# Performance work log

Hardware: AMD Instinct MI355X
Metric: run time of the kernel (lower is better)

Reference implementation:

```python
import jax, jax.numpy as jnp
import numpy as np

T, N, F_IN, F_HID, E = 12, 10000, 128, 128, 160000


def _gcn_norm(src, dst, ew, n):
    # PyG gcn_norm with add_self_loops=False: deg from edge_weight scattered at dst
    deg = jnp.zeros((n,), ew.dtype).at[dst].add(ew)
    dinv = jnp.where(deg > 0, jax.lax.rsqrt(jnp.where(deg > 0, deg, 1.0)), 0.0)
    return dinv[src] * ew * dinv[dst]


def _gcn(x, W, b, src, dst, norm, n):
    h = x @ W                                   # [n, out]
    out = jnp.zeros((n, W.shape[1]), h.dtype).at[dst].add(norm[:, None] * h[src])
    return out + b


def setup_inputs() -> dict:
    key = jax.random.key(0)
    ks = jax.random.split(key, 8)
    s = 1.0 / np.sqrt(F_IN)
    return {
        "x": jax.random.normal(ks[0], (T, N, F_IN), jnp.float32),
        "edge_index": jax.random.randint(ks[1], (2, E), 0, N, dtype=jnp.int64),
        "edge_weight": jax.random.uniform(ks[2], (E,), jnp.float32),
        "W1": jax.random.normal(ks[3], (F_IN, F_HID), jnp.float32) * s,
        "b1": jnp.zeros((F_HID,), jnp.float32),
        "W2": jax.random.normal(ks[4], (F_HID, F_IN), jnp.float32) * s,
        "b2": jnp.zeros((F_IN,), jnp.float32),
        "Wt1": jax.random.normal(ks[5], (F_IN, F_HID), jnp.float32) * s,
        "bt1": jnp.zeros((F_HID,), jnp.float32),
        "Wt2": jax.random.normal(ks[6], (F_HID, F_IN), jnp.float32) * s,
        "bt2": jnp.zeros((F_IN,), jnp.float32),
    }


def reference(x, edge_index, edge_weight, W1, b1, W2, b2, Wt1, bt1, Wt2, bt2):
    src, dst = edge_index[0], edge_index[1]
    norm = _gcn_norm(src, dst, edge_weight, N)

    def spatial(xt):  # [N, F_IN]
        h = jax.nn.relu(_gcn(xt, W1, b1, src, dst, norm, N))
        return _gcn(h, W2, b2, src, dst, norm, N)

    x = jax.vmap(spatial)(x)                    # [T, N, F_IN]

    # temporal block: bidirectional chain edges between consecutive time steps
    xf = x.reshape(T * N, F_IN)
    fwd = jnp.arange((T - 1) * N)
    tsrc = jnp.concatenate([fwd, fwd + N])
    tdst = jnp.concatenate([fwd + N, fwd])
    tw = jnp.ones(tsrc.shape, xf.dtype)
    tnorm = _gcn_norm(tsrc, tdst, tw, T * N)
    h = jax.nn.relu(_gcn(xf, Wt1, bt1, tsrc, tdst, tnorm, T * N))
    xf = _gcn(h, Wt2, bt2, tsrc, tdst, tnorm, T * N)
    x = xf.reshape(T, N, F_IN)

    return jnp.tanh(x)
```

## Files before the change

kernel.cpp:

```cpp
#include <hip/hip_runtime.h>
#include <hip/hip_bf16.h>
#include <hip/hip_fp16.h>

#define T_STEPS 12
#define N_NODES 10000
#define FDIM 128
#define M_ROWS (T_STEPS * N_NODES)

typedef __attribute__((ext_vector_type(8))) short short8v;
typedef __attribute__((ext_vector_type(8))) _Float16 half8v;
typedef __attribute__((ext_vector_type(2))) _Float16 half2v;
typedef __attribute__((ext_vector_type(4))) float f32x4;


__global__ __launch_bounds__(256) void k_count(const int* __restrict__ ei, int* __restrict__ cnt, int E) {
    int e = blockIdx.x * 256 + threadIdx.x;
    if (e < E) atomicAdd(&cnt[ei[E + e]], 1);
}

__global__ __launch_bounds__(1024) void k_scan(const int* __restrict__ cnt, int* __restrict__ rowptr,
                                               int* __restrict__ cursor) {
    __shared__ int buf[1024];
    __shared__ int base_s;
    int tid = threadIdx.x;
    if (tid == 0) base_s = 0;
    __syncthreads();
    for (int c0 = 0; c0 < N_NODES; c0 += 1024) {
        int i = c0 + tid;
        int x = (i < N_NODES) ? cnt[i] : 0;
        buf[tid] = x;
        __syncthreads();
        for (int off = 1; off < 1024; off <<= 1) {
            int v = (tid >= off) ? buf[tid - off] : 0;
            __syncthreads();
            buf[tid] += v;
            __syncthreads();
        }
        int excl = base_s + buf[tid] - x;
        if (i < N_NODES) { rowptr[i] = excl; cursor[i] = excl; }
        __syncthreads();
        if (tid == 0) base_s = base_s + buf[1023];
        __syncthreads();
    }
    if (tid == 0) rowptr[N_NODES] = base_s;
}

__global__ __launch_bounds__(256) void k_fill(const int* __restrict__ ei, const float* __restrict__ ew,
                                              int* __restrict__ cursor, uint2* __restrict__ epack, int E) {
    int e = blockIdx.x * 256 + threadIdx.x;
    if (e < E) {
        int s = ei[e];
        int d = ei[E + e];
        int slot = atomicAdd(&cursor[d], 1);
        epack[slot] = make_uint2((unsigned)s, __builtin_bit_cast(unsigned, ew[e]));
    }
}

__global__ __launch_bounds__(256) void k_dinv(const int* __restrict__ rowptr, const uint2* __restrict__ epack,
                                              float* __restrict__ dinv) {
    int n = blockIdx.x * 256 + threadIdx.x;
    if (n < N_NODES) {
        int r0 = rowptr[n], r1 = rowptr[n + 1];
        float s = 0.f;
        for (int i = r0; i < r1; ++i) s += __builtin_bit_cast(float, epack[i].y);
        dinv[n] = (s > 0.f) ? rsqrtf(s) : 0.f;
    }
}

__global__ __launch_bounds__(256) void k_scale(const int* __restrict__ rowptr, uint2* __restrict__ epack,
                                               const float* __restrict__ dinv) {
    int n = blockIdx.x * 256 + threadIdx.x;
    if (n < N_NODES) {
        int r0 = rowptr[n], r1 = rowptr[n + 1];
        float dn = dinv[n];
        for (int i = r0; i < r1; ++i) {
            uint2 e = epack[i];
            float v = dn * __builtin_bit_cast(float, e.y) * dinv[e.x];
            epack[i] = make_uint2(e.x * 256u, __builtin_bit_cast(unsigned, v));
        }
    }
}


__global__ __launch_bounds__(256) void k_wsplit4(const float* __restrict__ Wa, const float* __restrict__ Wb,
                                                 const float* __restrict__ Wc, const float* __restrict__ Wd,
                                                 short* __restrict__ base) {
    int wsel = blockIdx.y;
    const float* W = (wsel == 0) ? Wa : (wsel == 1) ? Wb : (wsel == 2) ? Wc : Wd;
    short* Whf = base + (size_t)wsel * 2 * FDIM * FDIM;
    short* Wlf = Whf + FDIM * FDIM;
    int idx = blockIdx.x * 256 + threadIdx.x;
    int k = idx >> 7, col = idx & 127;
    int s = k >> 5, kb = (k >> 3) & 3, j = k & 7;
    float w = W[(size_t)k * FDIM + col];
    _Float16 hi = (_Float16)w;
    _Float16 lo = (_Float16)(w - (float)hi);
    size_t oi = (size_t)(((s * 4 + kb) * 128 + col)) * 8 + j;
    Whf[oi] = __builtin_bit_cast(short, hi);
    Wlf[oi] = __builtin_bit_cast(short, lo);
}


template <typename IN_T, typename OUT_T>
__global__ __launch_bounds__(256) void k_gemm_f16(const IN_T* __restrict__ A,
                                                  const short* __restrict__ Whf,
                                                  const short* __restrict__ Wlf,
                                                  OUT_T* __restrict__ C, int Mrows) {
    int tid = threadIdx.x;
    int wave = tid >> 6, lane = tid & 63;
    int lr = lane & 15, kb = lane >> 4;
    int rbase = blockIdx.x * 128 + wave * 32;

    f32x4 acc[2][8];
#pragma unroll
    for (int m = 0; m < 2; ++m)
#pragma unroll
        for (int n = 0; n < 8; ++n) acc[m][n] = (f32x4){0.f, 0.f, 0.f, 0.f};

#pragma unroll
    for (int s = 0; s < 4; ++s) {
        half8v a[2];
#pragma unroll
        for (int m = 0; m < 2; ++m) {
            int r = rbase + m * 16 + lr;
            if (r > Mrows - 1) r = Mrows - 1;
            const IN_T* ap = &A[(size_t)r * FDIM + s * 32 + kb * 8];
            if constexpr (sizeof(IN_T) == 4) {
                float4 x0 = *(const float4*)ap;
                float4 x1 = *(const float4*)(ap + 4);
                a[m][0] = (_Float16)x0.x; a[m][1] = (_Float16)x0.y;
                a[m][2] = (_Float16)x0.z; a[m][3] = (_Float16)x0.w;
                a[m][4] = (_Float16)x1.x; a[m][5] = (_Float16)x1.y;
                a[m][6] = (_Float16)x1.z; a[m][7] = (_Float16)x1.w;
            } else {
                a[m] = __builtin_bit_cast(half8v, *(const short8v*)ap);
            }
        }
#pragma unroll
        for (int n = 0; n < 8; ++n) {
            size_t wo = (size_t)(((s * 4 + kb) * 128 + n * 16 + lr)) * 8;
            half8v wh = __builtin_bit_cast(half8v, *(const short8v*)&Whf[wo]);
            half8v wl = __builtin_bit_cast(half8v, *(const short8v*)&Wlf[wo]);
#pragma unroll
            for (int m = 0; m < 2; ++m) {
                acc[m][n] = __builtin_amdgcn_mfma_f32_16x16x32_f16(a[m], wh, acc[m][n], 0, 0, 0);
                acc[m][n] = __builtin_amdgcn_mfma_f32_16x16x32_f16(a[m], wl, acc[m][n], 0, 0, 0);
            }
        }
    }
#pragma unroll
    for (int m = 0; m < 2; ++m)
#pragma unroll
        for (int q = 0; q < 4; ++q) {
            int r = rbase + m * 16 + kb * 4 + q;
            if (r < Mrows) {
#pragma unroll
                for (int n = 0; n < 8; ++n)
                    C[(size_t)r * FDIM + n * 16 + lr] = (OUT_T)acc[m][n][q];
            }
        }
}


#define NPB 20
#define NB_HALF 250

__global__ __launch_bounds__(128) void k_aggx(const char* __restrict__ Sbytes,
                                              const int* __restrict__ rowptr,
                                              const uint2* __restrict__ epack,
                                              const float* __restrict__ bias, __half* __restrict__ out,
                                              int do_relu) {
    int bid = blockIdx.x;
    int x = bid & 7;
    int j = bid >> 3;
    int unit = j / NB_HALF;
    int nb = j - unit * NB_HALF;
    int t, n0;
    if (unit == 2) { t = 8 + (x >> 1); n0 = (x & 1) * 5000 + nb * NPB; }
    else           { t = x;            n0 = unit * 5000 + nb * NPB; }

    int wave = threadIdx.x >> 6, lane = threadIdx.x & 63;
    const char* St = Sbytes + (size_t)t * N_NODES * 256;
    unsigned lane4 = (unsigned)lane * 4u;
    float b0 = bias[2 * lane], b1 = bias[2 * lane + 1];

    int nbase = n0 + wave * (NPB / 2);
    for (int nn = 0; nn < NPB / 2; ++nn) {
        int n = nbase + nn;
        int r0 = __builtin_amdgcn_readfirstlane(rowptr[n]);
        int r1 = __builtin_amdgcn_readfirstlane(rowptr[n + 1]);
        float a0 = 0.f, a1 = 0.f;
        int i = r0;
        while (i + 16 <= r1) {
            unsigned sx[16]; float sv[16];
#pragma unroll
            for (int q = 0; q < 16; ++q) {
                uint2 e = epack[i + q];
                sx[q] = e.x;
                sv[q] = __builtin_bit_cast(float, e.y);
            }
            unsigned u[16];
#pragma unroll
            for (int q = 0; q < 16; ++q)
                u[q] = *(const unsigned*)(St + (sx[q] + lane4));
#pragma unroll
            for (int q = 0; q < 16; ++q) {
                half2v h = __builtin_bit_cast(half2v, u[q]);
                a0 = fmaf(sv[q], (float)h[0], a0);
                a1 = fmaf(sv[q], (float)h[1], a1);
            }
            i += 16;
        }
        while (i < r1) {
            unsigned sx[8]; float sv[8];
#pragma unroll
            for (int q = 0; q < 8; ++q) {
                int ii = i + q;
                int ic = (ii < r1) ? ii : r1 - 1;
                uint2 e = epack[ic];
                sx[q] = e.x;
                sv[q] = (ii < r1) ? __builtin_bit_cast(float, e.y) : 0.f;
            }
            unsigned u[8];
#pragma unroll
            for (int q = 0; q < 8; ++q)
                u[q] = *(const unsigned*)(St + (sx[q] + lane4));
#pragma unroll
            for (int q = 0; q < 8; ++q) {
                half2v h = __builtin_bit_cast(half2v, u[q]);
                a0 = fmaf(sv[q], (float)h[0], a0);
                a1 = fmaf(sv[q], (float)h[1], a1);
            }
            i += 8;
        }
        float o0 = a0 + b0, o1 = a1 + b1;
        if (do_relu) { o0 = fmaxf(o0, 0.f); o1 = fmaxf(o1, 0.f); }
        __half2 h = __floats2half2_rn(o0, o1);
        unsigned uo = __builtin_bit_cast(unsigned, h);
        __builtin_nontemporal_store(uo, (unsigned*)&out[((size_t)t * N_NODES + n) * FDIM + 2 * lane]);
    }
}


__device__ __forceinline__ void tagg_core(float2 (&s)[T_STEPS], float b0, float b1,
                                          float2 (&o)[T_STEPS]) {
    const float IS2 = 0.70710678118654752f;
#pragma unroll
    for (int t = 0; t < T_STEPS; ++t) {
        float dt = (t == 0 || t == T_STEPS - 1) ? 1.f : IS2;
        float a0 = 0.f, a1 = 0.f;
        if (t > 0) {
            float dp = (t - 1 == 0) ? 1.f : IS2;
            a0 += dp * s[t - 1].x; a1 += dp * s[t - 1].y;
        }
        if (t < T_STEPS - 1) {
            float dn = (t + 1 == T_STEPS - 1) ? 1.f : IS2;
            a0 += dn * s[t + 1].x; a1 += dn * s[t + 1].y;
        }
        o[t].x = dt * a0 + b0;
        o[t].y = dt * a1 + b1;
    }
}

__global__ __launch_bounds__(256) void k_tagg_relu(const __half2* __restrict__ S2,
                                                   const float* __restrict__ bias,
                                                   __half2* __restrict__ out) {
    int p = blockIdx.x * 256 + threadIdx.x;
    if (p >= N_NODES * 64) return;
    int c2 = p & 63;
    float b0 = bias[2 * c2], b1 = bias[2 * c2 + 1];
    float2 s[T_STEPS], o[T_STEPS];
#pragma unroll
    for (int t = 0; t < T_STEPS; ++t) s[t] = __half22float2(S2[(size_t)t * N_NODES * 64 + p]);
    tagg_core(s, b0, b1, o);
#pragma unroll
    for (int t = 0; t < T_STEPS; ++t) {
        float o0 = fmaxf(o[t].x, 0.f), o1 = fmaxf(o[t].y, 0.f);
        out[(size_t)t * N_NODES * 64 + p] = __floats2half2_rn(o0, o1);
    }
}

__global__ __launch_bounds__(256) void k_tagg_tanh(const __half2* __restrict__ S2,
                                                   const float* __restrict__ bias,
                                                   float* __restrict__ out) {
    int p = blockIdx.x * 256 + threadIdx.x;
    if (p >= N_NODES * 64) return;
    int c2 = p & 63;
    float b0 = bias[2 * c2], b1 = bias[2 * c2 + 1];
    float2 s[T_STEPS], o[T_STEPS];
#pragma unroll
    for (int t = 0; t < T_STEPS; ++t) s[t] = __half22float2(S2[(size_t)t * N_NODES * 64 + p]);
    tagg_core(s, b0, b1, o);
#pragma unroll
    for (int t = 0; t < T_STEPS; ++t) {
        float2 r = make_float2(tanhf(o[t].x), tanhf(o[t].y));
        *(float2*)&out[(size_t)t * N_NODES * FDIM + 2 * (size_t)p] = r;
    }
}


extern "C" void kernel_launch(void* const* d_in, const int* in_sizes, int n_in,
                              void* d_out, int out_size, void* d_ws, size_t ws_size,
                              hipStream_t stream) {
    const float* x   = (const float*)d_in[0];
    const int*   ei  = (const int*)d_in[1];
    const float* ew  = (const float*)d_in[2];
    const float* W1  = (const float*)d_in[3];
    const float* b1  = (const float*)d_in[4];
    const float* W2  = (const float*)d_in[5];
    const float* b2  = (const float*)d_in[6];
    const float* Wt1 = (const float*)d_in[7];
    const float* bt1 = (const float*)d_in[8];
    const float* Wt2 = (const float*)d_in[9];
    const float* bt2 = (const float*)d_in[10];
    float*  outF = (float*)d_out;
    __half* Sh   = (__half*)d_out;
    const int E = in_sizes[2];

    char* w = (char*)d_ws;
    __half* bufH = (__half*)w;
    size_t off   = (size_t)M_ROWS * FDIM * 2;
    __half* S2h  = (__half*)(w + off); off += (size_t)M_ROWS * FDIM * 2;
    int* cnt     = (int*)(w + off); off += (size_t)N_NODES * 4;
    int* rowptr  = (int*)(w + off); off += (size_t)(N_NODES + 1) * 4;
    int* cursor  = (int*)(w + off); off += (size_t)N_NODES * 4;
    uint2* epack = (uint2*)(w + off); off += (size_t)E * 8;
    float* dinv  = (float*)(w + off); off += (size_t)N_NODES * 4;
    short* Wsp   = (short*)(w + off); off += (size_t)8 * FDIM * FDIM * 2;
    const size_t WSZ = (size_t)FDIM * FDIM;
    short* W1h = Wsp;            short* W1l = Wsp + WSZ;
    short* W2h = Wsp + 2 * WSZ;  short* W2l = Wsp + 3 * WSZ;
    short* Wt1h = Wsp + 4 * WSZ; short* Wt1l = Wsp + 5 * WSZ;
    short* Wt2h = Wsp + 6 * WSZ; short* Wt2l = Wsp + 7 * WSZ;

    hipMemsetAsync(cnt, 0, (size_t)N_NODES * 4, stream);
    int eb = (E + 255) / 256;
    int nb = (N_NODES + 255) / 256;
    k_count<<<eb, 256, 0, stream>>>(ei, cnt, E);
    k_scan<<<1, 1024, 0, stream>>>(cnt, rowptr, cursor);
    k_fill<<<eb, 256, 0, stream>>>(ei, ew, cursor, epack, E);
    k_dinv<<<nb, 256, 0, stream>>>(rowptr, epack, dinv);
    k_scale<<<nb, 256, 0, stream>>>(rowptr, epack, dinv);

    dim3 wgrid((FDIM * FDIM) / 256, 4);
    k_wsplit4<<<wgrid, 256, 0, stream>>>(W1, W2, Wt1, Wt2, Wsp);

    int gb = (M_ROWS + 127) / 128;
    int tb = (N_NODES * 64 + 255) / 256;
    int ab = 8 * 3 * NB_HALF;

    k_gemm_f16<float, __half><<<gb, 256, 0, stream>>>(x, W1h, W1l, Sh, M_ROWS);
    k_aggx<<<ab, 128, 0, stream>>>((const char*)Sh, rowptr, epack, b1, bufH, 1);
    k_gemm_f16<__half, __half><<<gb, 256, 0, stream>>>(bufH, W2h, W2l, Sh, M_ROWS);
    k_aggx<<<ab, 128, 0, stream>>>((const char*)Sh, rowptr, epack, b2, bufH, 0);
    k_gemm_f16<__half, __half><<<gb, 256, 0, stream>>>(bufH, Wt1h, Wt1l, Sh, M_ROWS);
    k_tagg_relu<<<tb, 256, 0, stream>>>((const __half2*)Sh, bt1, (__half2*)bufH);
    k_gemm_f16<__half, __half><<<gb, 256, 0, stream>>>(bufH, Wt2h, Wt2l, S2h, M_ROWS);
    k_tagg_tanh<<<tb, 256, 0, stream>>>((const __half2*)S2h, bt2, outF);
}
```

Baseline: 298.8 us.

## Fuse temporal GEMMs with temporal aggregation using node-major layout

The second spatial aggregation now writes its output in node-major order ([N][T][F]), so each 120-row GEMM tile holds all 12 time steps for 10 nodes. A new k_gemm_tagg kernel runs the MFMA GEMM, stages the result in LDS, and applies the temporal chain aggregation with bias and relu or tanh in one pass. This removes the separate tagg kernels and the global round-trip of the intermediate result. The prefix scan is also replaced with a single-pass 256-thread chunked scan. The fused kernel adds LDS traffic and a synchronisation, and its last-stage output stores are strided by time step.

```diff
diff --git a/kernel.cpp b/kernel.cpp
--- a/kernel.cpp
+++ b/kernel.cpp
@@ -18,31 +18,37 @@
     if (e < E) atomicAdd(&cnt[ei[E + e]], 1);
 }
 
-__global__ __launch_bounds__(1024) void k_scan(const int* __restrict__ cnt, int* __restrict__ rowptr,
+__global__ __launch_bounds__(256) void k_scan2(const int* __restrict__ cnt, int* __restrict__ rowptr,
                                                int* __restrict__ cursor) {
-    __shared__ int buf[1024];
-    __shared__ int base_s;
+    __shared__ int part[256];
     int tid = threadIdx.x;
-    if (tid == 0) base_s = 0;
+    const int PER = 40;
+    int base = tid * PER;
+    int s = 0;
+#pragma unroll 8
+    for (int q = 0; q < PER; ++q) {
+        int idx = base + q;
+        s += (idx < N_NODES) ? cnt[idx] : 0;
+    }
+    part[tid] = s;
     __syncthreads();
-    for (int c0 = 0; c0 < N_NODES; c0 += 1024) {
-        int i = c0 + tid;
-        int x = (i < N_NODES) ? cnt[i] : 0;
-        buf[tid] = x;
+    for (int off = 1; off < 256; off <<= 1) {
+        int v = (tid >= off) ? part[tid - off] : 0;
         __syncthreads();
-        for (int off = 1; off < 1024; off <<= 1) {
-            int v = (tid >= off) ? buf[tid - off] : 0;
-            __syncthreads();
-            buf[tid] += v;
-            __syncthreads();
-        }
-        int excl = base_s + buf[tid] - x;
-        if (i < N_NODES) { rowptr[i] = excl; cursor[i] = excl; }
+        part[tid] += v;
         __syncthreads();
-        if (tid == 0) base_s = base_s + buf[1023];
-        __syncthreads();
-    }
-    if (tid == 0) rowptr[N_NODES] = base_s;
+    }
+    int run = (tid > 0) ? part[tid - 1] : 0;
+#pragma unroll 8
+    for (int q = 0; q < PER; ++q) {
+        int idx = base + q;
+        if (idx < N_NODES) {
+            rowptr[idx] = run;
+            cursor[idx] = run;
+            run += cnt[idx];
+        }
+    }
+    if (tid == 255) rowptr[N_NODES] = run;
 }
 
 __global__ __launch_bounds__(256) void k_fill(const int* __restrict__ ei, const float* __restrict__ ew,
@@ -162,6 +168,105 @@
 }
 
 
+template <int MODE, typename OUT_T>
+__global__ __launch_bounds__(256) void k_gemm_tagg(const __half* __restrict__ A,
+                                                   const short* __restrict__ Whf,
+                                                   const short* __restrict__ Wlf,
+                                                   const float* __restrict__ bias,
+                                                   OUT_T* __restrict__ out) {
+    __shared__ __half lds[128][132];
+    int tid = threadIdx.x;
+    int wave = tid >> 6, lane = tid & 63;
+    int lr = lane & 15, kb = lane >> 4;
+    int lbase = wave * 32;
+
+    f32x4 acc[2][8];
+#pragma unroll
+    for (int m = 0; m < 2; ++m)
+#pragma unroll
+        for (int n = 0; n < 8; ++n) acc[m][n] = (f32x4){0.f, 0.f, 0.f, 0.f};
+
+#pragma unroll
+    for (int s = 0; s < 4; ++s) {
+        half8v a[2];
+#pragma unroll
+        for (int m = 0; m < 2; ++m) {
+            int rl = lbase + m * 16 + lr;
+            if (rl > 119) rl = 119;
+            size_t r = (size_t)blockIdx.x * 120 + rl;
+            a[m] = __builtin_bit_cast(half8v, *(const short8v*)&A[r * FDIM + s * 32 + kb * 8]);
+        }
+#pragma unroll
+        for (int n = 0; n < 8; ++n) {
+            size_t wo = (size_t)(((s * 4 + kb) * 128 + n * 16 + lr)) * 8;
+            half8v wh = __builtin_bit_cast(half8v, *(const short8v*)&Whf[wo]);
+            half8v wl = __builtin_bit_cast(half8v, *(const short8v*)&Wlf[wo]);
+#pragma unroll
+            for (int m = 0; m < 2; ++m) {
+                acc[m][n] = __builtin_amdgcn_mfma_f32_16x16x32_f16(a[m], wh, acc[m][n], 0, 0, 0);
+                acc[m][n] = __builtin_amdgcn_mfma_f32_16x16x32_f16(a[m], wl, acc[m][n], 0, 0, 0);
+            }
+        }
+    }
+
+#pragma unroll
+    for (int m = 0; m < 2; ++m) {
+        int rowb = lbase + m * 16 + kb * 4;
+#pragma unroll
+        for (int n = 0; n < 8; ++n) {
+            int col = n * 16 + lr;
+            __half2 h01 = __floats2half2_rn(acc[m][n][0], acc[m][n][1]);
+            __half2 h23 = __floats2half2_rn(acc[m][n][2], acc[m][n][3]);
+            uint2 pk = make_uint2(__builtin_bit_cast(unsigned, h01), __builtin_bit_cast(unsigned, h23));
+            *(uint2*)&lds[col][rowb] = pk;
+        }
+    }
+    __syncthreads();
+
+    int f = tid & 127;
+    int g = tid >> 7;
+    float b = bias[f];
+    const float IS2 = 0.70710678118654752f;
+#pragma unroll
+    for (int it = 0; it < 5; ++it) {
+        int nd = g * 5 + it;
+        float sv[T_STEPS];
+#pragma unroll
+        for (int k = 0; k < 3; ++k) {
+            uint2 pk = *(const uint2*)&lds[f][nd * 12 + k * 4];
+            half2v p0 = __builtin_bit_cast(half2v, pk.x);
+            half2v p1 = __builtin_bit_cast(half2v, pk.y);
+            sv[k * 4 + 0] = (float)p0[0];
+            sv[k * 4 + 1] = (float)p0[1];
+            sv[k * 4 + 2] = (float)p1[0];
+            sv[k * 4 + 3] = (float)p1[1];
+        }
+        int gn = blockIdx.x * 10 + nd;
+#pragma unroll
+        for (int t = 0; t < T_STEPS; ++t) {
+            float dt = (t == 0 || t == T_STEPS - 1) ? 1.f : IS2;
+            float a = 0.f;
+            if (t > 0) {
+                float dp = (t - 1 == 0) ? 1.f : IS2;
+                a += dp * sv[t - 1];
+            }
+            if (t < T_STEPS - 1) {
+                float dn = (t + 1 == T_STEPS - 1) ? 1.f : IS2;
+                a += dn * sv[t + 1];
+            }
+            float o = dt * a + b;
+            if constexpr (MODE == 1) {
+                o = fmaxf(o, 0.f);
+                out[((size_t)gn * T_STEPS + t) * FDIM + f] = (OUT_T)o;
+            } else {
+                o = tanhf(o);
+                out[((size_t)t * N_NODES + gn) * FDIM + f] = (OUT_T)o;
+            }
+        }
+    }
+}
+
+
 #define NPB 20
 #define NB_HALF 250
 
@@ -169,7 +274,7 @@
                                               const int* __restrict__ rowptr,
                                               const uint2* __restrict__ epack,
                                               const float* __restrict__ bias, __half* __restrict__ out,
-                                              int do_relu) {
+                                              int do_relu, int out_nt) {
     int bid = blockIdx.x;
     int x = bid & 7;
     int j = bid >> 3;
@@ -237,64 +342,8 @@
         if (do_relu) { o0 = fmaxf(o0, 0.f); o1 = fmaxf(o1, 0.f); }
         __half2 h = __floats2half2_rn(o0, o1);
         unsigned uo = __builtin_bit_cast(unsigned, h);
-        __builtin_nontemporal_store(uo, (unsigned*)&out[((size_t)t * N_NODES + n) * FDIM + 2 * lane]);
-    }
-}
-
-
-__device__ __forceinline__ void tagg_core(float2 (&s)[T_STEPS], float b0, float b1,
-                                          float2 (&o)[T_STEPS]) {
-    const float IS2 = 0.70710678118654752f;
-#pragma unroll
-    for (int t = 0; t < T_STEPS; ++t) {
-        float dt = (t == 0 || t == T_STEPS - 1) ? 1.f : IS2;
-        float a0 = 0.f, a1 = 0.f;
-        if (t > 0) {
-            float dp = (t - 1 == 0) ? 1.f : IS2;
-            a0 += dp * s[t - 1].x; a1 += dp * s[t - 1].y;
-        }
-        if (t < T_STEPS - 1) {
-            float dn = (t + 1 == T_STEPS - 1) ? 1.f : IS2;
-            a0 += dn * s[t + 1].x; a1 += dn * s[t + 1].y;
-        }
-        o[t].x = dt * a0 + b0;
-        o[t].y = dt * a1 + b1;
-    }
-}
-
-__global__ __launch_bounds__(256) void k_tagg_relu(const __half2* __restrict__ S2,
-                                                   const float* __restrict__ bias,
-                                                   __half2* __restrict__ out) {
-    int p = blockIdx.x * 256 + threadIdx.x;
-    if (p >= N_NODES * 64) return;
-    int c2 = p & 63;
-    float b0 = bias[2 * c2], b1 = bias[2 * c2 + 1];
-    float2 s[T_STEPS], o[T_STEPS];
-#pragma unroll
-    for (int t = 0; t < T_STEPS; ++t) s[t] = __half22float2(S2[(size_t)t * N_NODES * 64 + p]);
-    tagg_core(s, b0, b1, o);
-#pragma unroll
-    for (int t = 0; t < T_STEPS; ++t) {
-        float o0 = fmaxf(o[t].x, 0.f), o1 = fmaxf(o[t].y, 0.f);
-        out[(size_t)t * N_NODES * 64 + p] = __floats2half2_rn(o0, o1);
-    }
-}
-
-__global__ __launch_bounds__(256) void k_tagg_tanh(const __half2* __restrict__ S2,
-                                                   const float* __restrict__ bias,
-                                                   float* __restrict__ out) {
-    int p = blockIdx.x * 256 + threadIdx.x;
-    if (p >= N_NODES * 64) return;
-    int c2 = p & 63;
-    float b0 = bias[2 * c2], b1 = bias[2 * c2 + 1];
-    float2 s[T_STEPS], o[T_STEPS];
-#pragma unroll
-    for (int t = 0; t < T_STEPS; ++t) s[t] = __half22float2(S2[(size_t)t * N_NODES * 64 + p]);
-    tagg_core(s, b0, b1, o);
-#pragma unroll
-    for (int t = 0; t < T_STEPS; ++t) {
-        float2 r = make_float2(tanhf(o[t].x), tanhf(o[t].y));
-        *(float2*)&out[(size_t)t * N_NODES * FDIM + 2 * (size_t)p] = r;
+        size_t orow = out_nt ? ((size_t)n * T_STEPS + t) : ((size_t)t * N_NODES + n);
+        __builtin_nontemporal_store(uo, (unsigned*)&out[orow * FDIM + 2 * lane]);
     }
 }
 
@@ -337,7 +386,7 @@
     int eb = (E + 255) / 256;
     int nb = (N_NODES + 255) / 256;
     k_count<<<eb, 256, 0, stream>>>(ei, cnt, E);
-    k_scan<<<1, 1024, 0, stream>>>(cnt, rowptr, cursor);
+    k_scan2<<<1, 256, 0, stream>>>(cnt, rowptr, cursor);
     k_fill<<<eb, 256, 0, stream>>>(ei, ew, cursor, epack, E);
     k_dinv<<<nb, 256, 0, stream>>>(rowptr, epack, dinv);
     k_scale<<<nb, 256, 0, stream>>>(rowptr, epack, dinv);
@@ -346,15 +395,13 @@
     k_wsplit4<<<wgrid, 256, 0, stream>>>(W1, W2, Wt1, Wt2, Wsp);
 
     int gb = (M_ROWS + 127) / 128;
-    int tb = (N_NODES * 64 + 255) / 256;
+    int fb = M_ROWS / 120;
     int ab = 8 * 3 * NB_HALF;
 
     k_gemm_f16<float, __half><<<gb, 256, 0, stream>>>(x, W1h, W1l, Sh, M_ROWS);
-    k_aggx<<<ab, 128, 0, stream>>>((const char*)Sh, rowptr, epack, b1, bufH, 1);
+    k_aggx<<<ab, 128, 0, stream>>>((const char*)Sh, rowptr, epack, b1, bufH, 1, 0);
     k_gemm_f16<__half, __half><<<gb, 256, 0, stream>>>(bufH, W2h, W2l, Sh, M_ROWS);
-    k_aggx<<<ab, 128, 0, stream>>>((const char*)Sh, rowptr, epack, b2, bufH, 0);
-    k_gemm_f16<__half, __half><<<gb, 256, 0, stream>>>(bufH, Wt1h, Wt1l, Sh, M_ROWS);
-    k_tagg_relu<<<tb, 256, 0, stream>>>((const __half2*)Sh, bt1, (__half2*)bufH);
-    k_gemm_f16<__half, __half><<<gb, 256, 0, stream>>>(bufH, Wt2h, Wt2l, S2h, M_ROWS);
-    k_tagg_tanh<<<tb, 256, 0, stream>>>((const __half2*)S2h, bt2, outF);
-}
+    k_aggx<<<ab, 128, 0, stream>>>((const char*)Sh, rowptr, epack, b2, bufH, 0, 1);
+    k_gemm_tagg<1, __half><<<fb, 256, 0, stream>>>(bufH, Wt1h, Wt1l, bt1, S2h);
+    k_gemm_tagg<2, float><<<fb, 256, 0, stream>>>(S2h, Wt2h, Wt2l, bt2, outF);
+}
```

Result: faster. 268.1 us (-10.3%).
